# Kernel tuning notes

Hardware: AMD Instinct MI355X
Metric: run time of the kernel (lower is better)

## Reference

```python
import jax, jax.numpy as jnp
import numpy as np

DEPTH = 30
IN_C, OUT_C, WIDTH = 1, 1, 1
DILATIONS = [i + 1 for i in range(10)]


def setup_inputs() -> dict:
    key = jax.random.key(0)
    ks = jax.random.split(key, 9)
    B, H, W = 4, 512, 512
    # MSDConvBlock weight init std from the source
    std = float(np.sqrt(2.0 / (9.0 * (IN_C + WIDTH * (DEPTH - 1)) + OUT_C)))
    x = jax.random.normal(ks[0], (B, IN_C, H, W), dtype=jnp.float32)
    # Wmsd[i, :i+1] are the 3x3 kernels at depth i: channel 0 acts on x,
    # channel z acts on hiddenstate z-1. Padded rows are unused.
    Wmsd = jax.random.normal(ks[1], (DEPTH, DEPTH, 3, 3), dtype=jnp.float32) * std
    bias = jax.random.normal(ks[2], (DEPTH,), dtype=jnp.float32) * 0.1  # shared per-depth bias
    # final 1x1 conv (zero-init in source; random here so the output is non-trivial)
    convW = jax.random.normal(ks[3], (OUT_C, WIDTH * DEPTH + IN_C, 1, 1), dtype=jnp.float32) * 0.1
    convB = jax.random.normal(ks[4], (OUT_C,), dtype=jnp.float32) * 0.1
    # ScalingBlocks: per-channel affine, identity init
    sin_w = jnp.ones((IN_C,), dtype=jnp.float32)
    sin_b = jnp.zeros((IN_C,), dtype=jnp.float32)
    sout_w = jnp.ones((OUT_C,), dtype=jnp.float32)
    sout_b = jnp.zeros((OUT_C,), dtype=jnp.float32)
    return {"x": x, "Wmsd": Wmsd, "bias": bias, "convW": convW, "convB": convB,
            "sin_w": sin_w, "sin_b": sin_b, "sout_w": sout_w, "sout_b": sout_b}


def _conv(x, w, dilation):
    # 'same' 3x3 dilated conv, NCHW / OIHW
    d = dilation
    return jax.lax.conv_general_dilated(
        x, w, window_strides=(1, 1), padding=[(d, d), (d, d)],
        rhs_dilation=(d, d), dimension_numbers=("NCHW", "OIHW", "NCHW"))


def reference(x, Wmsd, bias, convW, convB, sin_w, sin_b, sout_w, sout_b):
    depth = Wmsd.shape[0]
    x = x * sin_w[None, :, None, None] + sin_b[None, :, None, None]
    feats = x  # growing concat: [x, h0, h1, ...]
    for i in range(depth):
        d = DILATIONS[i % len(DILATIONS)]  # counter increments once per depth
        n_in = feats.shape[1]  # = IN_C + i (with width=1, IN_C=1)
        w = Wmsd[i, :n_in][None]  # [1, n_in, 3, 3]
        # sum of single-channel convs == one multi-channel conv over the concat
        h = _conv(feats, w, d)
        h = jax.nn.relu(h + bias[i])
        feats = jnp.concatenate([feats, h], axis=1)
    y = jax.lax.conv_general_dilated(
        feats, convW, window_strides=(1, 1), padding="VALID",
        dimension_numbers=("NCHW", "OIHW", "NCHW"))
    y = y + convB[None, :, None, None]
    y = y * sout_w[None, :, None, None] + sout_b[None, :, None, None]
    return y
```

## Files before the change

### kernel.cpp

```cpp
#include <hip/hip_runtime.h>


#define MSD_DEPTH 30
#define NB 4
#define IH 512
#define IW 512
#define HALO 16
#define WPp (IW + 2 * HALO)
#define HPp (IH + 2 * HALO)
#define PLANE_U ((size_t)WPp * HPp)
#define PSTR ((size_t)NB * PLANE_U)
#define NPAIR 15
#define NPIX (NB * IH * IW)
#define WPK_OFF ((size_t)20 << 20)
#define ZSTRIPS (32 * (WPp / 4) * NPAIR * NB)
#define SSTRIPS (512 * 8 * NPAIR * NB)
#define TOTZ (ZSTRIPS + SSTRIPS)

typedef _Float16 h2v __attribute__((ext_vector_type(2)));
typedef unsigned int u32;

__device__ __forceinline__ float fdot2u(u32 a, u32 b, float c) {
#if __has_builtin(__builtin_amdgcn_fdot2)
    return __builtin_amdgcn_fdot2(__builtin_bit_cast(h2v, a),
                                  __builtin_bit_cast(h2v, b), c, false);
#else
    h2v x = __builtin_bit_cast(h2v, a), y = __builtin_bit_cast(h2v, b);
    return c + (float)x[0] * (float)y[0] + (float)x[1] * (float)y[1];
#endif
}

__global__ __launch_bounds__(256) void preamble_kernel(const float* __restrict__ x,
                                                       const float* __restrict__ Wmsd,
                                                       const float* __restrict__ convW,
                                                       u32* __restrict__ feats,
                                                       u32* __restrict__ wpk,
                                                       u32* __restrict__ cpk,
                                                       const float* __restrict__ sw,
                                                       const float* __restrict__ sb) {
    int idx = blockIdx.x * 256 + threadIdx.x;

    if (idx < MSD_DEPTH * NPAIR * 9) {
        int I = idx / (NPAIR * 9);
        int rem = idx - I * (NPAIR * 9);
        int p = rem / 9, t = rem - p * 9;
        int NC = I + 1, c0 = 2 * p, c1 = 2 * p + 1;
        h2v pk;
        pk[0] = (_Float16)((c0 < NC) ? Wmsd[((size_t)I * MSD_DEPTH + c0) * 9 + t] : 0.f);
        pk[1] = (_Float16)((c1 < NC) ? Wmsd[((size_t)I * MSD_DEPTH + c1) * 9 + t] : 0.f);
        wpk[idx] = __builtin_bit_cast(u32, pk);
    }
    if (idx < NPAIR) {
        h2v pk;
        pk[0] = (_Float16)convW[2 * idx];
        pk[1] = (_Float16)convW[2 * idx + 1];
        cpk[idx] = __builtin_bit_cast(u32, pk);
    }

    if (idx < ZSTRIPS) {
        const int per = 32 * (WPp / 4);
        int sub = idx / per;
        int s = idx - sub * per;
        int rr = s / 136;
        int c4 = (s - rr * 136) * 4;
        int r = (rr < 16) ? rr : (IH + HALO) + (rr - 16);
        uint4 z = {0, 0, 0, 0};
        *(uint4*)(feats + (size_t)sub * PLANE_U + (size_t)r * WPp + c4) = z;
    } else if (idx < TOTZ) {
        int s = idx - ZSTRIPS;
        int sub = s >> 12;
        int rem = s & 4095;
        int r = HALO + (rem >> 3);
        int e = rem & 7;
        int c4 = (e < 4) ? (e * 4) : (IW + HALO + (e - 4) * 4);
        uint4 z = {0, 0, 0, 0};
        *(uint4*)(feats + (size_t)sub * PLANE_U + (size_t)r * WPp + c4) = z;
    }

    if (idx < NPIX / 8) {
        int pix = idx * 8;
        int b = pix >> 18;
        int y = (pix >> 9) & 511;
        int xx = pix & 511;
        const float sws = sw[0], sbs = sb[0];
        u32 v[8];
#pragma unroll
        for (int j = 0; j < 8; ++j) {
            _Float16 h = (_Float16)(x[pix + j] * sws + sbs);
            v[j] = (u32)__builtin_bit_cast(unsigned short, h);
        }
        u32* q = feats + (size_t)b * PLANE_U + (size_t)(y + HALO) * WPp + HALO + xx;
        *(uint4*)q = *(uint4*)&v[0];
        *(uint4*)(q + 4) = *(uint4*)&v[4];
    }
}

template <int I>
__global__ __launch_bounds__(128, 2) void depth_kernel(u32* __restrict__ feats,
                                                       const u32* __restrict__ wpk,
                                                       const u32* __restrict__ cpk,
                                                       const float* __restrict__ bias,
                                                       const float* __restrict__ convW,
                                                       const float* __restrict__ convB,
                                                       const float* __restrict__ soutw,
                                                       const float* __restrict__ soutb,
                                                       float* __restrict__ out) {
    constexpr int D = (I % 10) + 1;
    constexpr int NC = I + 1;
    constexpr int NP = (NC + 1) / 2;
    constexpr bool LAST = (I == MSD_DEPTH - 1);
    constexpr int C0 = (12 - D) >> 2;
    constexpr int C1 = (19 + D) >> 2;

    const int tid = threadIdx.x;
    const int widx = tid >> 6, lane = tid & 63;
    const int bid = blockIdx.x;
    const int xcd = bid & 7;
    const int kk = bid >> 3;
    const int b = xcd >> 1;
    const int y = (xcd & 1) * 256 + kk * 2 + widx;

    u32* const pb = feats + (size_t)b * PLANE_U + (size_t)(y + HALO) * WPp + HALO + lane * 8;

    float acc[8], ydot[8];
#pragma unroll
    for (int j = 0; j < 8; ++j) { acc[j] = 0.f; ydot[j] = 0.f; }

    const u32* const wrb = wpk + (size_t)I * (NPAIR * 9);

    u32 A[3][32], B[3][32];

    auto load_pair = [&](u32 (*bp)[32], int p) {
        const u32* pp = pb + (size_t)p * PSTR;
#pragma unroll
        for (int r = 0; r < 3; ++r) {
            const u32* rp = pp + (ptrdiff_t)(r - 1) * (D * WPp);
#pragma unroll
            for (int c = C0; c <= C1; ++c)
                *(uint4*)&bp[r][4 * c] = *(const uint4*)(rp - 12 + 4 * c);
        }
    };

    auto compute = [&](u32 (*bp)[32], int p) {
        const u32* wq = wrb + p * 9;
        const u32 cw = LAST ? cpk[p] : 0u;
#pragma unroll
        for (int r = 0; r < 3; ++r) {
            const u32* s = bp[r];
            const u32 w0 = wq[r * 3 + 0], w1 = wq[r * 3 + 1], w2 = wq[r * 3 + 2];
#pragma unroll
            for (int k = 0; k < 8; ++k) {
                float a = acc[k];
                a = fdot2u(s[12 - D + k], w0, a);
                a = fdot2u(s[12 + k],     w1, a);
                a = fdot2u(s[12 + D + k], w2, a);
                acc[k] = a;
            }
            if (LAST && r == 1) {
#pragma unroll
                for (int k = 0; k < 8; ++k) ydot[k] = fdot2u(s[12 + k], cw, ydot[k]);
            }
        }
    };

    load_pair(A, 0);
    int p = 0;
    for (; p + 2 <= NP; p += 2) {
        load_pair(B, p + 1);
        compute(A, p);
        if (p + 2 < NP) load_pair(A, p + 2);
        compute(B, p + 1);
    }
    if (p < NP) compute(A, p);

    const float b0 = bias[I];
    if (!LAST) {
        u32 part[8];
        if constexpr ((NC & 1) != 0) {
            const u32* rp = pb + (size_t)(NP - 1) * PSTR;
            *(uint4*)&part[0] = *(const uint4*)rp;
            *(uint4*)&part[4] = *(const uint4*)(rp + 4);
        }
        u32 mg[8];
#pragma unroll
        for (int j = 0; j < 8; ++j) {
            float h = acc[j] + b0;
            h = h > 0.f ? h : 0.f;
            u32 h16 = (u32)__builtin_bit_cast(unsigned short, (_Float16)h);
            if constexpr ((NC & 1) != 0)
                mg[j] = (part[j] & 0xFFFFu) | (h16 << 16);
            else
                mg[j] = h16;
        }
        u32* q = feats + (size_t)(NC >> 1) * PSTR + (size_t)b * PLANE_U +
                 (size_t)(y + HALO) * WPp + HALO + lane * 8;
        *(uint4*)q = *(uint4*)&mg[0];
        *(uint4*)(q + 4) = *(uint4*)&mg[4];
    } else {
        const float cw30 = convW[MSD_DEPTH];
        const float cb = convB[0], ow = soutw[0], ob = soutb[0];
        float* q = out + ((size_t)b * IH + y) * IW + lane * 8;
        float o[8];
#pragma unroll
        for (int j = 0; j < 8; ++j) {
            float h = acc[j] + b0;
            h = h > 0.f ? h : 0.f;
            float yv = ydot[j] + cw30 * h + cb;
            o[j] = yv * ow + ob;
        }
        *(uint4*)q = *(uint4*)&o[0];
        *(uint4*)(q + 4) = *(uint4*)&o[4];
    }
}

extern "C" void kernel_launch(void* const* d_in, const int* in_sizes, int n_in,
                              void* d_out, int out_size, void* d_ws, size_t ws_size,
                              hipStream_t stream) {
    const float* x     = (const float*)d_in[0];
    const float* Wmsd  = (const float*)d_in[1];
    const float* bias  = (const float*)d_in[2];
    const float* convW = (const float*)d_in[3];
    const float* convB = (const float*)d_in[4];
    const float* sinw  = (const float*)d_in[5];
    const float* sinb  = (const float*)d_in[6];
    const float* soutw = (const float*)d_in[7];
    const float* soutb = (const float*)d_in[8];
    float* out = (float*)d_out;

    u32* feats = (u32*)d_ws;
    u32* wpk = feats + WPK_OFF;
    u32* cpk = wpk + MSD_DEPTH * NPAIR * 9;

    preamble_kernel<<<(TOTZ + 255) / 256, 256, 0, stream>>>(x, Wmsd, convW,
                                                            feats, wpk, cpk,
                                                            sinw, sinb);

#define LNCH(I) depth_kernel<I><<<1024, 128, 0, stream>>>(feats, wpk, cpk, bias, convW, convB, soutw, soutb, out);
    LNCH(0)  LNCH(1)  LNCH(2)  LNCH(3)  LNCH(4)
    LNCH(5)  LNCH(6)  LNCH(7)  LNCH(8)  LNCH(9)
    LNCH(10) LNCH(11) LNCH(12) LNCH(13) LNCH(14)
    LNCH(15) LNCH(16) LNCH(17) LNCH(18) LNCH(19)
    LNCH(20) LNCH(21) LNCH(22) LNCH(23) LNCH(24)
    LNCH(25) LNCH(26) LNCH(27) LNCH(28) LNCH(29)
#undef LNCH
}
```

Before: 390.4 us.

## Fuse all depth layers into one cooperative kernel with grid barriers

Replaces the 30 per-depth kernel launches with a single cooperative persistent kernel that runs every depth phase and separates them with a hierarchical global atomic barrier followed by a cache invalidate. Rows whose dilated halo crosses into another XCD's region are read and written with system-scope atomics so they bypass non-coherent caches, and a fallback flag switches to always-coherent access if the block-to-XCC mapping is not the expected one. The goal is to remove launch overhead and inter-kernel drain gaps. In exchange it adds barrier latency, scalar atomic loads and stores on boundary rows, and depends on cooperative launch succeeding, with the old multi-kernel path kept as a fallback.

```diff
diff --git a/kernel.cpp b/kernel.cpp
--- a/kernel.cpp
+++ b/kernel.cpp
@@ -16,6 +16,8 @@
 #define ZSTRIPS (32 * (WPp / 4) * NPAIR * NB)
 #define SSTRIPS (512 * 8 * NPAIR * NB)
 #define TOTZ (ZSTRIPS + SSTRIPS)
+#define NBLK 1024
+#define TPB 128
 
 typedef _Float16 h2v __attribute__((ext_vector_type(2)));
 typedef unsigned int u32;
@@ -39,6 +41,8 @@
                                                        const float* __restrict__ sw,
                                                        const float* __restrict__ sb) {
     int idx = blockIdx.x * 256 + threadIdx.x;
+
+    if (idx < 64) wpk[8192 + idx] = 0u;
 
     if (idx < MSD_DEPTH * NPAIR * 9) {
         int I = idx / (NPAIR * 9);
@@ -96,6 +100,139 @@
 }
 
 template <int I>
+__device__ __forceinline__ void depth_body(int b, int y, int lane, bool safe,
+                                           u32* __restrict__ feats,
+                                           const u32* __restrict__ wpk,
+                                           const u32* __restrict__ cpk,
+                                           const float* __restrict__ bias,
+                                           const float* __restrict__ convW,
+                                           const float* __restrict__ convB,
+                                           const float* __restrict__ soutw,
+                                           const float* __restrict__ soutb,
+                                           float* __restrict__ out) {
+    constexpr int D = (I % 10) + 1;
+    constexpr int NC = I + 1;
+    constexpr int NP = (NC + 1) / 2;
+    constexpr bool LAST = (I == MSD_DEPTH - 1);
+    constexpr int C0 = (12 - D) >> 2;
+    constexpr int C1 = (19 + D) >> 2;
+
+    const int ybp = y & 255;
+    const bool xlo = safe ? (y >= D) : (y >= 256 && ybp < D);
+    const bool xhi = safe ? (y <= 511 - D) : (y < 256 && ybp >= 256 - D);
+
+    u32* const pb = feats + (size_t)b * PLANE_U + (size_t)(y + HALO) * WPp + HALO + lane * 8;
+
+    float acc[8], ydot[8];
+#pragma unroll
+    for (int j = 0; j < 8; ++j) { acc[j] = 0.f; ydot[j] = 0.f; }
+
+    const u32* const wrb = wpk + (size_t)I * (NPAIR * 9);
+
+    u32 A[3][32], B[3][32];
+
+    auto load_row = [&](u32* dst, const u32* rp, bool cross) {
+        if (cross) {
+#pragma unroll
+            for (int c = C0; c <= C1; ++c)
+#pragma unroll
+                for (int j = 0; j < 4; ++j)
+                    dst[4 * c + j] = __hip_atomic_load(
+                        (u32*)(rp - 12 + 4 * c + j), __ATOMIC_RELAXED,
+                        __HIP_MEMORY_SCOPE_SYSTEM);
+        } else {
+#pragma unroll
+            for (int c = C0; c <= C1; ++c)
+                *(uint4*)&dst[4 * c] = *(const uint4*)(rp - 12 + 4 * c);
+        }
+    };
+
+    auto load_pair = [&](u32 (*bp)[32], int p) {
+        const u32* pp = pb + (size_t)p * PSTR;
+        load_row(bp[0], pp - (ptrdiff_t)(D * WPp), xlo);
+        load_row(bp[1], pp, false);
+        load_row(bp[2], pp + (ptrdiff_t)(D * WPp), xhi);
+    };
+
+    auto compute = [&](u32 (*bp)[32], int p) {
+        const u32* wq = wrb + p * 9;
+        const u32 cw = LAST ? cpk[p] : 0u;
+#pragma unroll
+        for (int r = 0; r < 3; ++r) {
+            const u32* s = bp[r];
+            const u32 w0 = wq[r * 3 + 0], w1 = wq[r * 3 + 1], w2 = wq[r * 3 + 2];
+#pragma unroll
+            for (int k = 0; k < 8; ++k) {
+                float a = acc[k];
+                a = fdot2u(s[12 - D + k], w0, a);
+                a = fdot2u(s[12 + k],     w1, a);
+                a = fdot2u(s[12 + D + k], w2, a);
+                acc[k] = a;
+            }
+            if (LAST && r == 1) {
+#pragma unroll
+                for (int k = 0; k < 8; ++k) ydot[k] = fdot2u(s[12 + k], cw, ydot[k]);
+            }
+        }
+    };
+
+    load_pair(A, 0);
+    int p = 0;
+    for (; p + 2 <= NP; p += 2) {
+        load_pair(B, p + 1);
+        compute(A, p);
+        if (p + 2 < NP) load_pair(A, p + 2);
+        compute(B, p + 1);
+    }
+    if (p < NP) compute(A, p);
+
+    const float b0 = bias[I];
+    if (!LAST) {
+        u32 part[8];
+        if constexpr ((NC & 1) != 0) {
+            const u32* rp = pb + (size_t)(NP - 1) * PSTR;
+            *(uint4*)&part[0] = *(const uint4*)rp;
+            *(uint4*)&part[4] = *(const uint4*)(rp + 4);
+        }
+        u32 mg[8];
+#pragma unroll
+        for (int j = 0; j < 8; ++j) {
+            float h = acc[j] + b0;
+            h = h > 0.f ? h : 0.f;
+            u32 h16 = (u32)__builtin_bit_cast(unsigned short, (_Float16)h);
+            if constexpr ((NC & 1) != 0)
+                mg[j] = (part[j] & 0xFFFFu) | (h16 << 16);
+            else
+                mg[j] = h16;
+        }
+        u32* q = feats + (size_t)(NC >> 1) * PSTR + (size_t)b * PLANE_U +
+                 (size_t)(y + HALO) * WPp + HALO + lane * 8;
+        *(uint4*)q = *(uint4*)&mg[0];
+        *(uint4*)(q + 4) = *(uint4*)&mg[4];
+        if (safe || ybp >= 246 || ybp <= 9) {
+#pragma unroll
+            for (int j = 0; j < 8; ++j)
+                __hip_atomic_store(q + j, mg[j], __ATOMIC_RELAXED,
+                                   __HIP_MEMORY_SCOPE_SYSTEM);
+        }
+    } else {
+        const float cw30 = convW[MSD_DEPTH];
+        const float cb = convB[0], ow = soutw[0], ob = soutb[0];
+        float* q = out + ((size_t)b * IH + y) * IW + lane * 8;
+        float o[8];
+#pragma unroll
+        for (int j = 0; j < 8; ++j) {
+            float h = acc[j] + b0;
+            h = h > 0.f ? h : 0.f;
+            float yv = ydot[j] + cw30 * h + cb;
+            o[j] = yv * ow + ob;
+        }
+        *(uint4*)q = *(uint4*)&o[0];
+        *(uint4*)(q + 4) = *(uint4*)&o[4];
+    }
+}
+
+template <int I>
 __global__ __launch_bounds__(128, 2) void depth_kernel(u32* __restrict__ feats,
                                                        const u32* __restrict__ wpk,
                                                        const u32* __restrict__ cpk,
@@ -105,112 +242,76 @@
                                                        const float* __restrict__ soutw,
                                                        const float* __restrict__ soutb,
                                                        float* __restrict__ out) {
-    constexpr int D = (I % 10) + 1;
-    constexpr int NC = I + 1;
-    constexpr int NP = (NC + 1) / 2;
-    constexpr bool LAST = (I == MSD_DEPTH - 1);
-    constexpr int C0 = (12 - D) >> 2;
-    constexpr int C1 = (19 + D) >> 2;
-
     const int tid = threadIdx.x;
     const int widx = tid >> 6, lane = tid & 63;
     const int bid = blockIdx.x;
     const int xcd = bid & 7;
-    const int kk = bid >> 3;
     const int b = xcd >> 1;
-    const int y = (xcd & 1) * 256 + kk * 2 + widx;
-
-    u32* const pb = feats + (size_t)b * PLANE_U + (size_t)(y + HALO) * WPp + HALO + lane * 8;
-
-    float acc[8], ydot[8];
-#pragma unroll
-    for (int j = 0; j < 8; ++j) { acc[j] = 0.f; ydot[j] = 0.f; }
-
-    const u32* const wrb = wpk + (size_t)I * (NPAIR * 9);
-
-    u32 A[3][32], B[3][32];
-
-    auto load_pair = [&](u32 (*bp)[32], int p) {
-        const u32* pp = pb + (size_t)p * PSTR;
-#pragma unroll
-        for (int r = 0; r < 3; ++r) {
-            const u32* rp = pp + (ptrdiff_t)(r - 1) * (D * WPp);
-#pragma unroll
-            for (int c = C0; c <= C1; ++c)
-                *(uint4*)&bp[r][4 * c] = *(const uint4*)(rp - 12 + 4 * c);
-        }
-    };
-
-    auto compute = [&](u32 (*bp)[32], int p) {
-        const u32* wq = wrb + p * 9;
-        const u32 cw = LAST ? cpk[p] : 0u;
-#pragma unroll
-        for (int r = 0; r < 3; ++r) {
-            const u32* s = bp[r];
-            const u32 w0 = wq[r * 3 + 0], w1 = wq[r * 3 + 1], w2 = wq[r * 3 + 2];
-#pragma unroll
-            for (int k = 0; k < 8; ++k) {
-                float a = acc[k];
-                a = fdot2u(s[12 - D + k], w0, a);
-                a = fdot2u(s[12 + k],     w1, a);
-                a = fdot2u(s[12 + D + k], w2, a);
-                acc[k] = a;
-            }
-            if (LAST && r == 1) {
-#pragma unroll
-                for (int k = 0; k < 8; ++k) ydot[k] = fdot2u(s[12 + k], cw, ydot[k]);
-            }
-        }
-    };
-
-    load_pair(A, 0);
-    int p = 0;
-    for (; p + 2 <= NP; p += 2) {
-        load_pair(B, p + 1);
-        compute(A, p);
-        if (p + 2 < NP) load_pair(A, p + 2);
-        compute(B, p + 1);
-    }
-    if (p < NP) compute(A, p);
-
-    const float b0 = bias[I];
-    if (!LAST) {
-        u32 part[8];
-        if constexpr ((NC & 1) != 0) {
-            const u32* rp = pb + (size_t)(NP - 1) * PSTR;
-            *(uint4*)&part[0] = *(const uint4*)rp;
-            *(uint4*)&part[4] = *(const uint4*)(rp + 4);
-        }
-        u32 mg[8];
-#pragma unroll
-        for (int j = 0; j < 8; ++j) {
-            float h = acc[j] + b0;
-            h = h > 0.f ? h : 0.f;
-            u32 h16 = (u32)__builtin_bit_cast(unsigned short, (_Float16)h);
-            if constexpr ((NC & 1) != 0)
-                mg[j] = (part[j] & 0xFFFFu) | (h16 << 16);
-            else
-                mg[j] = h16;
-        }
-        u32* q = feats + (size_t)(NC >> 1) * PSTR + (size_t)b * PLANE_U +
-                 (size_t)(y + HALO) * WPp + HALO + lane * 8;
-        *(uint4*)q = *(uint4*)&mg[0];
-        *(uint4*)(q + 4) = *(uint4*)&mg[4];
-    } else {
-        const float cw30 = convW[MSD_DEPTH];
-        const float cb = convB[0], ow = soutw[0], ob = soutb[0];
-        float* q = out + ((size_t)b * IH + y) * IW + lane * 8;
-        float o[8];
-#pragma unroll
-        for (int j = 0; j < 8; ++j) {
-            float h = acc[j] + b0;
-            h = h > 0.f ? h : 0.f;
-            float yv = ydot[j] + cw30 * h + cb;
-            o[j] = yv * ow + ob;
-        }
-        *(uint4*)q = *(uint4*)&o[0];
-        *(uint4*)(q + 4) = *(uint4*)&o[4];
-    }
+    const int y = (xcd & 1) * 256 + (bid >> 3) * 2 + widx;
+    depth_body<I>(b, y, lane, false, feats, wpk, cpk, bias, convW, convB,
+                  soutw, soutb, out);
+}
+
+__device__ __forceinline__ void gbar(u32* bars, u32 n) {
+    asm volatile("" ::: "memory");
+    __syncthreads();
+    if (threadIdx.x == 0) {
+        u32 old = __hip_atomic_fetch_add(&bars[blockIdx.x >> 5], 1u,
+                                         __ATOMIC_RELAXED, __HIP_MEMORY_SCOPE_AGENT);
+        if (old == n * 32u - 1u)
+            __hip_atomic_fetch_add(&bars[32], 1u, __ATOMIC_RELAXED,
+                                   __HIP_MEMORY_SCOPE_AGENT);
+        while (__hip_atomic_load(&bars[32], __ATOMIC_RELAXED,
+                                 __HIP_MEMORY_SCOPE_SYSTEM) < n * 32u)
+            __builtin_amdgcn_s_sleep(2);
+    }
+    __syncthreads();
+    asm volatile("buffer_inv" ::: "memory");
+    __builtin_amdgcn_sched_barrier(0);
+}
+
+__global__ __launch_bounds__(TPB, 2) void msd_fused(u32* __restrict__ feats,
+                                                    const u32* __restrict__ wpk,
+                                                    const u32* __restrict__ cpk,
+                                                    const float* __restrict__ bias,
+                                                    const float* __restrict__ convW,
+                                                    const float* __restrict__ convB,
+                                                    const float* __restrict__ soutw,
+                                                    const float* __restrict__ soutb,
+                                                    float* __restrict__ out,
+                                                    u32* __restrict__ bars) {
+    const int tid = threadIdx.x;
+    const int widx = tid >> 6, lane = tid & 63;
+    const int bid = blockIdx.x;
+    const int xcd = bid & 7;
+    const int b = xcd >> 1;
+    const int y = (xcd & 1) * 256 + (bid >> 3) * 2 + widx;
+
+    if (tid == 0) {
+        u32 xcc;
+        asm volatile("s_getreg_b32 %0, hwreg(HW_REG_XCC_ID)" : "=s"(xcc));
+        if ((int)(xcc & 7u) != xcd)
+            __hip_atomic_store(&bars[33], 1u, __ATOMIC_RELAXED,
+                               __HIP_MEMORY_SCOPE_SYSTEM);
+    }
+    gbar(bars, 1);
+    const bool safe = __hip_atomic_load(&bars[33], __ATOMIC_RELAXED,
+                                        __HIP_MEMORY_SCOPE_SYSTEM) != 0;
+
+#define PH(I, n)                                                               \
+    depth_body<I>(b, y, lane, safe, feats, wpk, cpk, bias, convW, convB,       \
+                  soutw, soutb, out);                                          \
+    gbar(bars, n);
+
+    PH(0, 2)   PH(1, 3)   PH(2, 4)   PH(3, 5)   PH(4, 6)
+    PH(5, 7)   PH(6, 8)   PH(7, 9)   PH(8, 10)  PH(9, 11)
+    PH(10, 12) PH(11, 13) PH(12, 14) PH(13, 15) PH(14, 16)
+    PH(15, 17) PH(16, 18) PH(17, 19) PH(18, 20) PH(19, 21)
+    PH(20, 22) PH(21, 23) PH(22, 24) PH(23, 25) PH(24, 26)
+    PH(25, 27) PH(26, 28) PH(27, 29) PH(28, 30)
+#undef PH
+    depth_body<29>(b, y, lane, safe, feats, wpk, cpk, bias, convW, convB,
+                   soutw, soutb, out);
 }
 
 extern "C" void kernel_launch(void* const* d_in, const int* in_sizes, int n_in,
@@ -230,17 +331,25 @@
     u32* feats = (u32*)d_ws;
     u32* wpk = feats + WPK_OFF;
     u32* cpk = wpk + MSD_DEPTH * NPAIR * 9;
+    u32* bars = wpk + 8192;
 
     preamble_kernel<<<(TOTZ + 255) / 256, 256, 0, stream>>>(x, Wmsd, convW,
                                                             feats, wpk, cpk,
                                                             sinw, sinb);
 
+    void* args[] = {&feats, &wpk, &cpk, &bias, &convW, &convB,
+                    &soutw, &soutb, &out, &bars};
+    hipError_t rc = hipLaunchCooperativeKernel(msd_fused, dim3(NBLK), dim3(TPB),
+                                               args, 0u, stream);
+    if (rc != hipSuccess) {
+        (void)hipGetLastError();
 #define LNCH(I) depth_kernel<I><<<1024, 128, 0, stream>>>(feats, wpk, cpk, bias, convW, convB, soutw, soutb, out);
-    LNCH(0)  LNCH(1)  LNCH(2)  LNCH(3)  LNCH(4)
-    LNCH(5)  LNCH(6)  LNCH(7)  LNCH(8)  LNCH(9)
-    LNCH(10) LNCH(11) LNCH(12) LNCH(13) LNCH(14)
-    LNCH(15) LNCH(16) LNCH(17) LNCH(18) LNCH(19)
-    LNCH(20) LNCH(21) LNCH(22) LNCH(23) LNCH(24)
-    LNCH(25) LNCH(26) LNCH(27) LNCH(28) LNCH(29)
+        LNCH(0)  LNCH(1)  LNCH(2)  LNCH(3)  LNCH(4)
+        LNCH(5)  LNCH(6)  LNCH(7)  LNCH(8)  LNCH(9)
+        LNCH(10) LNCH(11) LNCH(12) LNCH(13) LNCH(14)
+        LNCH(15) LNCH(16) LNCH(17) LNCH(18) LNCH(19)
+        LNCH(20) LNCH(21) LNCH(22) LNCH(23) LNCH(24)
+        LNCH(25) LNCH(26) LNCH(27) LNCH(28) LNCH(29)
 #undef LNCH
-}
+    }
+}
```

After: 1.403 ms. 259% more time.

## Halve per-thread pixel count and widen blocks to raise occupancy

Applied to the files above, without the earlier changes.

Each thread now computes 4 output pixels instead of 8, and each 512-thread block covers four full rows split into half-row waves. This shrinks the register buffers, and the launch bounds are raised to 512 threads with 4 blocks per CU, so more waves are resident to hide memory latency. The odd-channel merge now takes the partner half-word from the already-loaded center row instead of re-reading global memory. The cost is more redundant halo loading per output pixel, because each thread's window is narrower relative to the dilation.

```diff
diff --git a/kernel.cpp b/kernel.cpp
--- a/kernel.cpp
+++ b/kernel.cpp
@@ -96,7 +96,7 @@
 }
 
 template <int I>
-__global__ __launch_bounds__(128, 2) void depth_kernel(u32* __restrict__ feats,
+__global__ __launch_bounds__(512, 4) void depth_kernel(u32* __restrict__ feats,
                                                        const u32* __restrict__ wpk,
                                                        const u32* __restrict__ cpk,
                                                        const float* __restrict__ bias,
@@ -110,7 +110,8 @@
     constexpr int NP = (NC + 1) / 2;
     constexpr bool LAST = (I == MSD_DEPTH - 1);
     constexpr int C0 = (12 - D) >> 2;
-    constexpr int C1 = (19 + D) >> 2;
+    constexpr int C1 = (15 + D) >> 2;
+    constexpr int BW = 4 * (C1 + 1);
 
     const int tid = threadIdx.x;
     const int widx = tid >> 6, lane = tid & 63;
@@ -118,30 +119,34 @@
     const int xcd = bid & 7;
     const int kk = bid >> 3;
     const int b = xcd >> 1;
-    const int y = (xcd & 1) * 256 + kk * 2 + widx;
-
-    u32* const pb = feats + (size_t)b * PLANE_U + (size_t)(y + HALO) * WPp + HALO + lane * 8;
-
-    float acc[8], ydot[8];
-#pragma unroll
-    for (int j = 0; j < 8; ++j) { acc[j] = 0.f; ydot[j] = 0.f; }
+    const int y = (xcd & 1) * 256 + kk * 4 + (widx >> 1);
+    const int h = widx & 1;
+    const int xx = h * 256 + lane * 4;
+
+    u32* const pb = feats + (size_t)b * PLANE_U + (size_t)(y + HALO) * WPp + HALO + xx;
+
+    float acc[4], ydot[4];
+#pragma unroll
+    for (int j = 0; j < 4; ++j) { acc[j] = 0.f; ydot[j] = 0.f; }
 
     const u32* const wrb = wpk + (size_t)I * (NPAIR * 9);
 
-    u32 A[3][32], B[3][32];
-
-    auto load_pair = [&](u32 (*bp)[32], int p) {
+    u32 A[3][BW], B[3][BW];
+
+    auto load_row = [&](u32* dst, const u32* rp) {
+#pragma unroll
+        for (int c = C0; c <= C1; ++c)
+            *(uint4*)&dst[4 * c] = *(const uint4*)(rp - 12 + 4 * c);
+    };
+
+    auto load_pair = [&](u32 (*bp)[BW], int p) {
         const u32* pp = pb + (size_t)p * PSTR;
-#pragma unroll
-        for (int r = 0; r < 3; ++r) {
-            const u32* rp = pp + (ptrdiff_t)(r - 1) * (D * WPp);
-#pragma unroll
-            for (int c = C0; c <= C1; ++c)
-                *(uint4*)&bp[r][4 * c] = *(const uint4*)(rp - 12 + 4 * c);
-        }
+        load_row(bp[0], pp - (ptrdiff_t)(D * WPp));
+        load_row(bp[1], pp);
+        load_row(bp[2], pp + (ptrdiff_t)(D * WPp));
     };
 
-    auto compute = [&](u32 (*bp)[32], int p) {
+    auto compute = [&](u32 (*bp)[BW], int p) {
         const u32* wq = wrb + p * 9;
         const u32 cw = LAST ? cpk[p] : 0u;
 #pragma unroll
@@ -149,7 +154,7 @@
             const u32* s = bp[r];
             const u32 w0 = wq[r * 3 + 0], w1 = wq[r * 3 + 1], w2 = wq[r * 3 + 2];
 #pragma unroll
-            for (int k = 0; k < 8; ++k) {
+            for (int k = 0; k < 4; ++k) {
                 float a = acc[k];
                 a = fdot2u(s[12 - D + k], w0, a);
                 a = fdot2u(s[12 + k],     w1, a);
@@ -158,7 +163,7 @@
             }
             if (LAST && r == 1) {
 #pragma unroll
-                for (int k = 0; k < 8; ++k) ydot[k] = fdot2u(s[12 + k], cw, ydot[k]);
+                for (int k = 0; k < 4; ++k) ydot[k] = fdot2u(s[12 + k], cw, ydot[k]);
             }
         }
     };
@@ -175,41 +180,40 @@
 
     const float b0 = bias[I];
     if (!LAST) {
-        u32 part[8];
+        u32 part[4];
         if constexpr ((NC & 1) != 0) {
-            const u32* rp = pb + (size_t)(NP - 1) * PSTR;
-            *(uint4*)&part[0] = *(const uint4*)rp;
-            *(uint4*)&part[4] = *(const uint4*)(rp + 4);
-        }
-        u32 mg[8];
-#pragma unroll
-        for (int j = 0; j < 8; ++j) {
-            float h = acc[j] + b0;
-            h = h > 0.f ? h : 0.f;
-            u32 h16 = (u32)__builtin_bit_cast(unsigned short, (_Float16)h);
+            constexpr bool inA = (((NP - 1) & 1) == 0);
+            const u32* s = inA ? A[1] : B[1];
+#pragma unroll
+            for (int j = 0; j < 4; ++j) part[j] = s[12 + j];
+        }
+        u32 mg[4];
+#pragma unroll
+        for (int j = 0; j < 4; ++j) {
+            float hh = acc[j] + b0;
+            hh = hh > 0.f ? hh : 0.f;
+            u32 h16 = (u32)__builtin_bit_cast(unsigned short, (_Float16)hh);
             if constexpr ((NC & 1) != 0)
                 mg[j] = (part[j] & 0xFFFFu) | (h16 << 16);
             else
                 mg[j] = h16;
         }
         u32* q = feats + (size_t)(NC >> 1) * PSTR + (size_t)b * PLANE_U +
-                 (size_t)(y + HALO) * WPp + HALO + lane * 8;
+                 (size_t)(y + HALO) * WPp + HALO + xx;
         *(uint4*)q = *(uint4*)&mg[0];
-        *(uint4*)(q + 4) = *(uint4*)&mg[4];
     } else {
         const float cw30 = convW[MSD_DEPTH];
         const float cb = convB[0], ow = soutw[0], ob = soutb[0];
-        float* q = out + ((size_t)b * IH + y) * IW + lane * 8;
-        float o[8];
-#pragma unroll
-        for (int j = 0; j < 8; ++j) {
-            float h = acc[j] + b0;
-            h = h > 0.f ? h : 0.f;
-            float yv = ydot[j] + cw30 * h + cb;
+        float* q = out + ((size_t)b * IH + y) * IW + xx;
+        float o[4];
+#pragma unroll
+        for (int j = 0; j < 4; ++j) {
+            float hh = acc[j] + b0;
+            hh = hh > 0.f ? hh : 0.f;
+            float yv = ydot[j] + cw30 * hh + cb;
             o[j] = yv * ow + ob;
         }
         *(uint4*)q = *(uint4*)&o[0];
-        *(uint4*)(q + 4) = *(uint4*)&o[4];
     }
 }
 
@@ -235,7 +239,7 @@
                                                             feats, wpk, cpk,
                                                             sinw, sinb);
 
-#define LNCH(I) depth_kernel<I><<<1024, 128, 0, stream>>>(feats, wpk, cpk, bias, convW, convB, soutw, soutb, out);
+#define LNCH(I) depth_kernel<I><<<512, 512, 0, stream>>>(feats, wpk, cpk, bias, convW, convB, soutw, soutb, out);
     LNCH(0)  LNCH(1)  LNCH(2)  LNCH(3)  LNCH(4)
     LNCH(5)  LNCH(6)  LNCH(7)  LNCH(8)  LNCH(9)
     LNCH(10) LNCH(11) LNCH(12) LNCH(13) LNCH(14)
```

Measured after the change: 380.6 us. 1.03x faster.

## Add 4-pixel-per-thread kernel for small dilations and interleave row-level prefetch

Applied to the files above, without the earlier changes.

For layers with dilation up to 4, the launcher now uses a new kernel that computes 4 pixels per thread with 512-thread blocks and smaller register tiles. The goal is more parallelism and occupancy with less halo over-fetch. Both kernels now prefetch row by row, interleaved with compute, instead of whole pairs, and reuse the odd-channel partial word from registers rather than reloading it from global memory. The risks are more redundant halo loads per output pixel in the 4-wide variant and different register pressure.

```diff
diff --git a/kernel.cpp b/kernel.cpp
--- a/kernel.cpp
+++ b/kernel.cpp
@@ -96,15 +96,15 @@
 }
 
 template <int I>
-__global__ __launch_bounds__(128, 2) void depth_kernel(u32* __restrict__ feats,
-                                                       const u32* __restrict__ wpk,
-                                                       const u32* __restrict__ cpk,
-                                                       const float* __restrict__ bias,
-                                                       const float* __restrict__ convW,
-                                                       const float* __restrict__ convB,
-                                                       const float* __restrict__ soutw,
-                                                       const float* __restrict__ soutb,
-                                                       float* __restrict__ out) {
+__global__ __launch_bounds__(128, 2) void depth8_kernel(u32* __restrict__ feats,
+                                                        const u32* __restrict__ wpk,
+                                                        const u32* __restrict__ cpk,
+                                                        const float* __restrict__ bias,
+                                                        const float* __restrict__ convW,
+                                                        const float* __restrict__ convB,
+                                                        const float* __restrict__ soutw,
+                                                        const float* __restrict__ soutb,
+                                                        float* __restrict__ out) {
     constexpr int D = (I % 10) + 1;
     constexpr int NC = I + 1;
     constexpr int NP = (NC + 1) / 2;
@@ -130,56 +130,58 @@
 
     u32 A[3][32], B[3][32];
 
+    auto load_row = [&](u32* dst, int p, int r) {
+        const u32* rp = pb + (size_t)p * PSTR + (ptrdiff_t)((r - 1) * (D * WPp));
+#pragma unroll
+        for (int c = C0; c <= C1; ++c)
+            *(uint4*)&dst[4 * c] = *(const uint4*)(rp - 12 + 4 * c);
+    };
     auto load_pair = [&](u32 (*bp)[32], int p) {
-        const u32* pp = pb + (size_t)p * PSTR;
-#pragma unroll
-        for (int r = 0; r < 3; ++r) {
-            const u32* rp = pp + (ptrdiff_t)(r - 1) * (D * WPp);
-#pragma unroll
-            for (int c = C0; c <= C1; ++c)
-                *(uint4*)&bp[r][4 * c] = *(const uint4*)(rp - 12 + 4 * c);
-        }
-    };
-
-    auto compute = [&](u32 (*bp)[32], int p) {
+        load_row(bp[0], p, 0); load_row(bp[1], p, 1); load_row(bp[2], p, 2);
+    };
+    auto compute_r = [&](const u32* s, int p, int r) {
         const u32* wq = wrb + p * 9;
-        const u32 cw = LAST ? cpk[p] : 0u;
-#pragma unroll
-        for (int r = 0; r < 3; ++r) {
-            const u32* s = bp[r];
-            const u32 w0 = wq[r * 3 + 0], w1 = wq[r * 3 + 1], w2 = wq[r * 3 + 2];
-#pragma unroll
-            for (int k = 0; k < 8; ++k) {
-                float a = acc[k];
-                a = fdot2u(s[12 - D + k], w0, a);
-                a = fdot2u(s[12 + k],     w1, a);
-                a = fdot2u(s[12 + D + k], w2, a);
-                acc[k] = a;
-            }
-            if (LAST && r == 1) {
-#pragma unroll
-                for (int k = 0; k < 8; ++k) ydot[k] = fdot2u(s[12 + k], cw, ydot[k]);
-            }
+        const u32 w0 = wq[r * 3 + 0], w1 = wq[r * 3 + 1], w2 = wq[r * 3 + 2];
+#pragma unroll
+        for (int k = 0; k < 8; ++k) {
+            float a = acc[k];
+            a = fdot2u(s[12 - D + k], w0, a);
+            a = fdot2u(s[12 + k],     w1, a);
+            a = fdot2u(s[12 + D + k], w2, a);
+            acc[k] = a;
+        }
+        if (LAST && r == 1) {
+            const u32 cw = cpk[p];
+#pragma unroll
+            for (int k = 0; k < 8; ++k) ydot[k] = fdot2u(s[12 + k], cw, ydot[k]);
         }
     };
 
     load_pair(A, 0);
+    if constexpr (NP >= 2) load_pair(B, 1);
     int p = 0;
     for (; p + 2 <= NP; p += 2) {
-        load_pair(B, p + 1);
-        compute(A, p);
-        if (p + 2 < NP) load_pair(A, p + 2);
-        compute(B, p + 1);
-    }
-    if (p < NP) compute(A, p);
+#pragma unroll
+        for (int r = 0; r < 3; ++r) {
+            compute_r(A[r], p, r);
+            if (p + 2 < NP) load_row(A[r], p + 2, r);
+        }
+#pragma unroll
+        for (int r = 0; r < 3; ++r) {
+            compute_r(B[r], p + 1, r);
+            if (p + 3 < NP) load_row(B[r], p + 3, r);
+        }
+    }
+    if (p < NP) { compute_r(A[0], p, 0); compute_r(A[1], p, 1); compute_r(A[2], p, 2); }
 
     const float b0 = bias[I];
     if (!LAST) {
         u32 part[8];
         if constexpr ((NC & 1) != 0) {
-            const u32* rp = pb + (size_t)(NP - 1) * PSTR;
-            *(uint4*)&part[0] = *(const uint4*)rp;
-            *(uint4*)&part[4] = *(const uint4*)(rp + 4);
+            constexpr bool inA = (((NP - 1) & 1) == 0);
+            const u32* s = inA ? A[1] : B[1];
+#pragma unroll
+            for (int j = 0; j < 8; ++j) part[j] = s[12 + j];
         }
         u32 mg[8];
 #pragma unroll
@@ -210,6 +212,126 @@
         }
         *(uint4*)q = *(uint4*)&o[0];
         *(uint4*)(q + 4) = *(uint4*)&o[4];
+    }
+}
+
+template <int I>
+__global__ __launch_bounds__(512, 4) void depth4_kernel(u32* __restrict__ feats,
+                                                        const u32* __restrict__ wpk,
+                                                        const u32* __restrict__ cpk,
+                                                        const float* __restrict__ bias,
+                                                        const float* __restrict__ convW,
+                                                        const float* __restrict__ convB,
+                                                        const float* __restrict__ soutw,
+                                                        const float* __restrict__ soutb,
+                                                        float* __restrict__ out) {
+    constexpr int D = (I % 10) + 1;
+    constexpr int NC = I + 1;
+    constexpr int NP = (NC + 1) / 2;
+    constexpr bool LAST = (I == MSD_DEPTH - 1);
+    constexpr int C0 = (12 - D) >> 2;
+    constexpr int C1 = (15 + D) >> 2;
+
+    const int tid = threadIdx.x;
+    const int widx = tid >> 6, lane = tid & 63;
+    const int bid = blockIdx.x;
+    const int xcd = bid & 7;
+    const int kk = bid >> 3;
+    const int b = xcd >> 1;
+    const int y = (xcd & 1) * 256 + kk * 4 + (widx >> 1);
+    const int h = widx & 1;
+    const int xx = h * 256 + lane * 4;
+
+    u32* const pb = feats + (size_t)b * PLANE_U + (size_t)(y + HALO) * WPp + HALO + xx;
+
+    float acc[4], ydot[4];
+#pragma unroll
+    for (int j = 0; j < 4; ++j) { acc[j] = 0.f; ydot[j] = 0.f; }
+
+    const u32* const wrb = wpk + (size_t)I * (NPAIR * 9);
+
+    u32 A[3][20], B[3][20];
+
+    auto load_row = [&](u32* dst, int p, int r) {
+        const u32* rp = pb + (size_t)p * PSTR + (ptrdiff_t)((r - 1) * (D * WPp));
+#pragma unroll
+        for (int c = C0; c <= C1; ++c)
+            *(uint4*)&dst[4 * c] = *(const uint4*)(rp - 12 + 4 * c);
+    };
+    auto load_pair = [&](u32 (*bp)[20], int p) {
+        load_row(bp[0], p, 0); load_row(bp[1], p, 1); load_row(bp[2], p, 2);
+    };
+    auto compute_r = [&](const u32* s, int p, int r) {
+        const u32* wq = wrb + p * 9;
+        const u32 w0 = wq[r * 3 + 0], w1 = wq[r * 3 + 1], w2 = wq[r * 3 + 2];
+#pragma unroll
+        for (int k = 0; k < 4; ++k) {
+            float a = acc[k];
+            a = fdot2u(s[12 - D + k], w0, a);
+            a = fdot2u(s[12 + k],     w1, a);
+            a = fdot2u(s[12 + D + k], w2, a);
+            acc[k] = a;
+        }
+        if (LAST && r == 1) {
+            const u32 cw = cpk[p];
+#pragma unroll
+            for (int k = 0; k < 4; ++k) ydot[k] = fdot2u(s[12 + k], cw, ydot[k]);
+        }
+    };
+
+    load_pair(A, 0);
+    if constexpr (NP >= 2) load_pair(B, 1);
+    int p = 0;
+    for (; p + 2 <= NP; p += 2) {
+#pragma unroll
+        for (int r = 0; r < 3; ++r) {
+            compute_r(A[r], p, r);
+            if (p + 2 < NP) load_row(A[r], p + 2, r);
+        }
+#pragma unroll
+        for (int r = 0; r < 3; ++r) {
+            compute_r(B[r], p + 1, r);
+            if (p + 3 < NP) load_row(B[r], p + 3, r);
+        }
+    }
+    if (p < NP) { compute_r(A[0], p, 0); compute_r(A[1], p, 1); compute_r(A[2], p, 2); }
+
+    const float b0 = bias[I];
+    if (!LAST) {
+        u32 part[4];
+        if constexpr ((NC & 1) != 0) {
+            constexpr bool inA = (((NP - 1) & 1) == 0);
+            const u32* s = inA ? A[1] : B[1];
+#pragma unroll
+            for (int j = 0; j < 4; ++j) part[j] = s[12 + j];
+        }
+        u32 mg[4];
+#pragma unroll
+        for (int j = 0; j < 4; ++j) {
+            float hh = acc[j] + b0;
+            hh = hh > 0.f ? hh : 0.f;
+            u32 h16 = (u32)__builtin_bit_cast(unsigned short, (_Float16)hh);
+            if constexpr ((NC & 1) != 0)
+                mg[j] = (part[j] & 0xFFFFu) | (h16 << 16);
+            else
+                mg[j] = h16;
+        }
+        u32* q = feats + (size_t)(NC >> 1) * PSTR + (size_t)b * PLANE_U +
+                 (size_t)(y + HALO) * WPp + HALO + xx;
+        *(uint4*)q = *(uint4*)&mg[0];
+    } else {
+        const float cw30 = convW[MSD_DEPTH];
+        const float cb = convB[0], ow = soutw[0], ob = soutb[0];
+        float* q = out + ((size_t)b * IH + y) * IW + xx;
+        float o[4];
+#pragma unroll
+        for (int j = 0; j < 4; ++j) {
+            float hh = acc[j] + b0;
+            hh = hh > 0.f ? hh : 0.f;
+            float yv = ydot[j] + cw30 * hh + cb;
+            o[j] = yv * ow + ob;
+        }
+        *(uint4*)q = *(uint4*)&o[0];
     }
 }
 
@@ -235,7 +357,17 @@
                                                             feats, wpk, cpk,
                                                             sinw, sinb);
 
-#define LNCH(I) depth_kernel<I><<<1024, 128, 0, stream>>>(feats, wpk, cpk, bias, convW, convB, soutw, soutb, out);
+#define LNCH(I)                                                                     \
+    do {                                                                            \
+        if ((I % 10) + 1 <= 4)                                                      \
+            depth4_kernel<I><<<512, 512, 0, stream>>>(feats, wpk, cpk, bias,        \
+                                                      convW, convB, soutw, soutb,   \
+                                                      out);                         \
+        else                                                                        \
+            depth8_kernel<I><<<1024, 128, 0, stream>>>(feats, wpk, cpk, bias,       \
+                                                       convW, convB, soutw, soutb,  \
+                                                       out);                        \
+    } while (0);
     LNCH(0)  LNCH(1)  LNCH(2)  LNCH(3)  LNCH(4)
     LNCH(5)  LNCH(6)  LNCH(7)  LNCH(8)  LNCH(9)
     LNCH(10) LNCH(11) LNCH(12) LNCH(13) LNCH(14)
```

Result: slower. 766.1 us (+96.3%).
